# Kernel tuning notes

Hardware: AMD Instinct MI355X
Metric: run time of the kernel (lower is better)

The kernel has to match this reference:

```python
import jax, jax.numpy as jnp
import numpy as np

DIM, DFF, NH = 768, 2048, 12
HD = DIM // NH
N, NOBJ, L = 16, 52, 24
EPS = 1e-5


def setup_inputs() -> dict:
    key = jax.random.key(0)
    ks = jax.random.split(key, 16)
    g = lambda k, shape: jax.random.normal(k, shape, jnp.float32) * 0.02
    inp = {
        "lang": jax.random.normal(ks[0], (N, L, DIM), jnp.float32),
        "obj": jax.random.normal(ks[1], (N, NOBJ, DIM), jnp.float32),
        "lang_mask": jnp.ones((N, L), jnp.int32),
        "obj_mask": jnp.ones((N, NOBJ), jnp.int32),
        "co_mask": jnp.ones((N, L, NOBJ), jnp.int32),
    }
    # two multi-head attention blocks (edge / node): q,k,v,o projections
    for i, nm in enumerate(["e_wq", "e_wk", "e_wv", "e_wo", "n_wq", "n_wk", "n_wv", "n_wo"]):
        inp[nm] = g(ks[2 + i], (DIM, DIM))
        inp[nm.replace("w", "b")] = jnp.zeros((DIM,), jnp.float32)
    inp["ffn_w1"] = g(ks[10], (2 * DIM, DFF)); inp["ffn_b1"] = jnp.zeros((DFF,), jnp.float32)
    inp["ffn_w2"] = g(ks[11], (DFF, DIM)); inp["ffn_b2"] = jnp.zeros((DIM,), jnp.float32)
    for nm in ["ln_e", "ln_q", "ln2"]:
        inp[nm + "_g"] = jnp.ones((DIM,), jnp.float32)
        inp[nm + "_b"] = jnp.zeros((DIM,), jnp.float32)
    return inp


def _layernorm(x, g, b):
    m = jnp.mean(x, -1, keepdims=True)
    v = jnp.mean((x - m) ** 2, -1, keepdims=True)
    return (x - m) * jax.lax.rsqrt(v + EPS) * g + b


def _fwd(lang, obj, co_mask,
         e_wq, e_bq, e_wk, e_bk, e_wv, e_bv, e_wo, e_bo,
         n_wq, n_bq, n_wk, n_bk, n_wv, n_bv, n_wo, n_bo,
         ffn_w1, ffn_b1, ffn_w2, ffn_b2,
         ln_e_g, ln_e_b, ln_q_g, ln_q_b, ln2_g, ln2_b):
    scale = jnp.float32(1.0 / np.sqrt(HD))
    co_t = co_mask.swapaxes(1, 2)  # [N, nobj, L]: query objects attend over lang keys

    # ---- node branch: standard cross-attention obj -> lang ----
    qh = (obj @ n_wq + n_bq).reshape(N, NOBJ, NH, HD)
    kh = (lang @ n_wk + n_bk).reshape(N, L, NH, HD)
    vh = (lang @ n_wv + n_bv).reshape(N, L, NH, HD)
    s = jnp.einsum('nqhd,nlhd->nhql', qh, kh) * scale  # [N,H,nobj,L]
    s = jnp.where(co_t[:, None, :, :] > 0, s, jnp.float32(-1e9))
    a = jax.nn.softmax(s, axis=-1)
    node = jnp.einsum('nhql,nlhd->nqhd', a, vh).reshape(N, NOBJ, DIM) @ n_wo + n_bo

    # ---- edge branch: pairwise diffs attend over lang, then max over partner ----
    diff = obj[:, :, None, :] - obj[:, None, :, :]            # [N,i,j,D]
    qhe = (diff @ e_wq + e_bq).reshape(N, NOBJ, NOBJ, NH, HD)
    khe = (lang @ e_wk + e_bk).reshape(N, L, NH, HD)
    vhe = (lang @ e_wv + e_bv).reshape(N, L, NH, HD)
    se = jnp.einsum('nijhd,nlhd->nhijl', qhe, khe) * scale    # [N,H,i,j,L]
    # mask depends on (n, j, l): torch repeats co_mask^T over the i batch dim
    se = jnp.where(co_t[:, None, None, :, :] > 0, se, jnp.float32(-1e9))
    ae = jax.nn.softmax(se, axis=-1)
    oe = jnp.einsum('nhijl,nlhd->nijhd', ae, vhe).reshape(N, NOBJ, NOBJ, DIM)
    oe = oe @ e_wo + e_bo                                      # [N,i,j,D]
    edge = jnp.max(oe, axis=2)                                 # max over query/partner j -> [N,i,D]

    # ---- fuse ----
    xe = _layernorm(obj + edge, ln_e_g, ln_e_b)
    xn = _layernorm(obj + node, ln_q_g, ln_q_b)
    h = jnp.concatenate((xn, xe), -1)
    h = jax.nn.relu(h @ ffn_w1 + ffn_b1) @ ffn_w2 + ffn_b2
    return _layernorm(xn + h, ln2_g, ln2_b)


def reference(lang, obj, lang_mask, obj_mask, co_mask,
              e_wq, e_bq, e_wk, e_bk, e_wv, e_bv, e_wo, e_bo,
              n_wq, n_bq, n_wk, n_bk, n_wv, n_bv, n_wo, n_bo,
              ffn_w1, ffn_b1, ffn_w2, ffn_b2,
              ln_e_g, ln_e_b, ln_q_g, ln_q_b, ln2_g, ln2_b):
    return _fwd(lang, obj, co_mask,
                e_wq, e_bq, e_wk, e_bk, e_wv, e_bv, e_wo, e_bo,
                n_wq, n_bq, n_wk, n_bk, n_wv, n_bv, n_wo, n_bo,
                ffn_w1, ffn_b1, ffn_w2, ffn_b2,
                ln_e_g, ln_e_b, ln_q_g, ln_q_b, ln2_g, ln2_b)
```

## Files before the change

### kernel.cpp

```cpp
#include <hip/hip_runtime.h>
#include <math.h>

#define NOBJ 52
#define LL 24
#define NHEAD 12

typedef __attribute__((ext_vector_type(8))) short bf16x8;
typedef __attribute__((ext_vector_type(4))) float f32x4;
typedef __attribute__((ext_vector_type(4))) unsigned int u32x4;
typedef __attribute__((ext_vector_type(2))) unsigned int u32x2;

__device__ __forceinline__ unsigned short f2b(float x) {
    union { float f; unsigned int u; } v; v.f = x;
    unsigned int r = v.u + 0x7fffu + ((v.u >> 16) & 1u);
    return (unsigned short)(r >> 16);
}
__device__ __forceinline__ float b2f(unsigned short u) {
    union { unsigned int u; float f; } v; v.u = ((unsigned int)u) << 16;
    return v.f;
}
__device__ __forceinline__ unsigned int pack2(float a, float b) {
    return (unsigned int)f2b(a) | ((unsigned int)f2b(b) << 16);
}
__device__ __forceinline__ f32x4 mfma16(bf16x8 a, bf16x8 b, f32x4 c) {
    return __builtin_amdgcn_mfma_f32_16x16x32_bf16(a, b, c, 0, 0, 0);
}
__device__ __forceinline__ void gl_lds16(const void* g, void* lds) {
    __builtin_amdgcn_global_load_lds(
        (const __attribute__((address_space(1))) unsigned int*)g,
        (__attribute__((address_space(3))) unsigned int*)lds, 16, 0, 0);
}

__device__ __forceinline__ void transpose_tile(const float* __restrict__ src,
    unsigned short* __restrict__ dst, int K, int N, int t, char* smem)
{
    float (*ts)[65] = (float(*)[65])smem;
    const int tid = threadIdx.x;
    const int ntk = K >> 6;
    const int k0 = (t % ntk) << 6, n0 = (t / ntk) << 6;
    const int tx = tid & 63, ty = tid >> 6;
    #pragma unroll
    for (int i2 = 0; i2 < 16; ++i2) {
        const int row = i2 * 4 + ty;
        ts[row][tx] = src[(size_t)(k0 + row) * N + n0 + tx];
    }
    __syncthreads();
    #pragma unroll
    for (int i2 = 0; i2 < 16; ++i2) {
        const int row = i2 * 4 + ty;
        dst[(size_t)(n0 + row) * K + k0 + tx] = f2b(ts[tx][row]);
    }
}

__global__ __launch_bounds__(256)
void pack1_kernel(const float* s0, const float* s1, const float* s2,
                  const float* s3, const float* s4, const float* s5,
                  const float* s6, const float* s7,
                  unsigned short* d0, unsigned short* d1, unsigned short* d2,
                  unsigned short* d3, unsigned short* d4, unsigned short* d5,
                  unsigned short* d6, unsigned short* d7,
                  const float* obj, const float* lang, const float* n_bq,
                  const float* e_bk, const float* e_bv,
                  const float* n_bk, const float* n_bv,
                  unsigned short* objb, unsigned short* langb,
                  float* bqc, float* blc)
{
    __shared__ __align__(16) char smem[16640];
    const int bid = blockIdx.x;
    const int tid = threadIdx.x;
    if (bid < 1152) {
        const int job = bid / 144, t = bid % 144;
        const float* src; unsigned short* dst;
        switch (job) {
            case 0: src = s0; dst = d0; break;
            case 1: src = s1; dst = d1; break;
            case 2: src = s2; dst = d2; break;
            case 3: src = s3; dst = d3; break;
            case 4: src = s4; dst = d4; break;
            case 5: src = s5; dst = d5; break;
            case 6: src = s6; dst = d6; break;
            default: src = s7; dst = d7; break;
        }
        transpose_tile(src, dst, 768, 768, t, smem);
    } else {
        const int base = ((bid - 1152) * 256 + tid) * 4;
        const int T0 = 638976, T1 = 933888, T2 = 935424, T3 = 938496;
        if (base >= T3) return;
        if (base < T0) {
            f32x4 v = *(const f32x4*)(obj + base);
            *(u32x2*)(objb + base) = (u32x2){pack2(v[0], v[1]), pack2(v[2], v[3])};
        } else if (base < T1) {
            const int j = base - T0;
            f32x4 v = *(const f32x4*)(lang + j);
            *(u32x2*)(langb + j) = (u32x2){pack2(v[0], v[1]), pack2(v[2], v[3])};
        } else if (base < T2) {
            const int j = base - T1;
            if (j < 768) { *(f32x4*)(bqc + j) = (f32x4){0.f, 0.f, 0.f, 0.f}; }
            else         { *(f32x4*)(bqc + j) = *(const f32x4*)(n_bq + j - 768); }
        } else {
            const int j = base - T2;
            const int s = j / 768, c = j % 768;
            const float* p = (s == 0) ? e_bk : (s == 1) ? e_bv : (s == 2) ? n_bk : n_bv;
            *(f32x4*)(blc + j) = *(const f32x4*)(p + c);
        }
    }
}

struct GemmJob {
    const unsigned short* A; const unsigned short* Bt; const float* bias;
    float* C; unsigned short* Cb;
    int lda, ldb, ldc, K, nbx, nb, relu, swz;
};

__device__ __forceinline__ void gemm_body(const GemmJob J, int bid, char* smem)
{
    unsigned short* As = (unsigned short*)smem;
    unsigned short* Bs = (unsigned short*)(smem + 16384);
    int bx, by;
    if (J.swz) {
        const int cpx = J.nb >> 3;
        const int gid = (bid & 7) * cpx + (bid >> 3);
        const int nbm = J.nb / J.nbx;
        bx = gid / nbm; by = gid % nbm;
    } else { bx = bid % J.nbx; by = bid / J.nbx; }
    const int n0 = bx * 128, m0 = by * 64;
    const int tid = threadIdx.x;
    const int lane = tid & 63;
    const int w = tid >> 6, wr = w >> 1, wc = w & 1;
    const int lr = lane & 15, lk = lane >> 4;
    const int lda = J.lda, ldb = J.ldb, K = J.K;
    const unsigned short* Ab = J.A + (size_t)m0 * lda;
    const unsigned short* Bb = J.Bt + (size_t)n0 * ldb;

    f32x4 acc[2][4] = {};
    const int NT = K >> 6;

    #pragma unroll
    for (int q = 0; q < 2; ++q) {
        const int c = q * 256 + tid, row = c >> 3, p = (c & 7) ^ (row & 7);
        gl_lds16(Ab + (size_t)row * lda + p * 8, As + c * 8);
    }
    #pragma unroll
    for (int q = 0; q < 4; ++q) {
        const int c = q * 256 + tid, row = c >> 3, p = (c & 7) ^ (row & 7);
        gl_lds16(Bb + (size_t)row * ldb + p * 8, Bs + c * 8);
    }
    __syncthreads();

    for (int t = 0; t < NT; ++t) {
        const int cur = t & 1;
        if (t + 1 < NT) {
            const int k0 = (t + 1) << 6;
            #pragma unroll
            for (int q = 0; q < 2; ++q) {
                const int c = q * 256 + tid, row = c >> 3, p = (c & 7) ^ (row & 7);
                gl_lds16(Ab + (size_t)row * lda + k0 + p * 8, As + (cur ^ 1) * 4096 + c * 8);
            }
            #pragma unroll
            for (int q = 0; q < 4; ++q) {
                const int c = q * 256 + tid, row = c >> 3, p = (c & 7) ^ (row & 7);
                gl_lds16(Bb + (size_t)row * ldb + k0 + p * 8, Bs + (cur ^ 1) * 8192 + c * 8);
            }
        }
        #pragma unroll
        for (int kk = 0; kk < 2; ++kk) {
            bf16x8 af[2], bv[4];
            #pragma unroll
            for (int mt = 0; mt < 2; ++mt) {
                const int row = wr * 32 + mt * 16 + lr;
                const int pc = (kk * 4 + lk) ^ (row & 7);
                af[mt] = *(const bf16x8*)(As + cur * 4096 + row * 64 + pc * 8);
            }
            #pragma unroll
            for (int nt = 0; nt < 4; ++nt) {
                const int col = wc * 64 + nt * 16 + lr;
                const int pc = (kk * 4 + lk) ^ (col & 7);
                bv[nt] = *(const bf16x8*)(Bs + cur * 8192 + col * 64 + pc * 8);
            }
            #pragma unroll
            for (int mt = 0; mt < 2; ++mt)
                #pragma unroll
                for (int nt = 0; nt < 4; ++nt)
                    acc[mt][nt] = mfma16(af[mt], bv[nt], acc[mt][nt]);
        }
        __syncthreads();
    }

    #pragma unroll
    for (int mt = 0; mt < 2; ++mt) {
        #pragma unroll
        for (int nt = 0; nt < 4; ++nt) {
            const int col = n0 + wc * 64 + nt * 16 + lr;
            const float bvv = J.bias ? J.bias[col] : 0.f;
            #pragma unroll
            for (int r = 0; r < 4; ++r) {
                const int row = m0 + wr * 32 + mt * 16 + lk * 4 + r;
                float v = acc[mt][nt][r] + bvv;
                if (J.relu) v = fmaxf(v, 0.f);
                if (J.C)  J.C[(size_t)row * J.ldc + col] = v;
                if (J.Cb) J.Cb[(size_t)row * J.ldc + col] = f2b(v);
            }
        }
    }
}

__global__ __launch_bounds__(256)
void gemm_tn4(GemmJob j0, GemmJob j1, GemmJob j2, GemmJob j3)
{
    __shared__ __align__(16) char smem[49152];
    int bid = blockIdx.x;
    if (bid < j0.nb) { gemm_body(j0, bid, smem); return; }
    bid -= j0.nb;
    if (bid < j1.nb) { gemm_body(j1, bid, smem); return; }
    bid -= j1.nb;
    if (bid < j2.nb) { gemm_body(j2, bid, smem); return; }
    bid -= j2.nb;
    gemm_body(j3, bid, smem);
}

__global__ __launch_bounds__(256)
void proj_pack_kernel(GemmJob j0, GemmJob j1,
                      const float* w1, const float* w2,
                      unsigned short* W1t, unsigned short* W2t)
{
    __shared__ __align__(16) char smem[49152];
    int bid = blockIdx.x;
    if (bid < j0.nb) { gemm_body(j0, bid, smem); return; }
    bid -= j0.nb;
    if (bid < j1.nb) { gemm_body(j1, bid, smem); return; }
    const int t = bid - j1.nb;
    if (t < 768) transpose_tile(w1, W1t, 1536, 2048, t, smem);
    else transpose_tile(w2, W2t, 2048, 768, t - 768, smem);
}

__global__ __launch_bounds__(256)
void mid3_kernel(const unsigned short* __restrict__ QCb,
                 const unsigned short* __restrict__ LCb,
                 const unsigned short* __restrict__ Wet,
                 const unsigned short* __restrict__ Wot,
                 const float* __restrict__ e_bq,
                 unsigned short* __restrict__ VWe,
                 unsigned short* __restrict__ VWn,
                 float* __restrict__ S2e, float* __restrict__ Tb,
                 float* __restrict__ S2n)
{
    __shared__ __align__(16) union USm {
        struct { unsigned short As[8192], Bs[8192]; } g;
        unsigned short Ct[128 * 136];
        struct { float sA[52][68], sB[24][68]; } s;
    } U;
    const int bid = blockIdx.x;
    const int tid = threadIdx.x;

    if (bid < 432) {
        const int sub = bid >= 216;
        const int b = sub ? bid - 216 : bid;
        const int aoff = sub ? 2304 : 768;
        const unsigned short* Bt = sub ? Wot : Wet;
        unsigned short* Vout = sub ? VWn : VWe;

        const int h = b / 18, rm = b % 18, mt = rm / 6, ntile = rm % 6;
        const int m0 = mt * 128, n0 = ntile * 128;
        const int lane = tid & 63, w = tid >> 6, wr = w >> 1, wc = w & 1;
        const int lr = lane & 15, lk = lane >> 4;
        #pragma unroll
        for (int q = 0; q < 4; ++q) {
            const int c = q * 256 + tid, row = c >> 3, p = (c & 7) ^ (row & 7);
            gl_lds16(LCb + (size_t)(m0 + row) * 3072 + aoff + h * 64 + p * 8, &U.g.As[c * 8]);
            gl_lds16(Bt + (size_t)(n0 + row) * 768 + h * 64 + p * 8, &U.g.Bs[c * 8]);
        }
        __syncthreads();
        f32x4 acc[4][4] = {};
        #pragma unroll
        for (int kk = 0; kk < 2; ++kk) {
            bf16x8 af[4], bv[4];
            #pragma unroll
            for (int m2 = 0; m2 < 4; ++m2) {
                const int row = wr * 64 + m2 * 16 + lr;
                const int pc = (kk * 4 + lk) ^ (row & 7);
                af[m2] = *(const bf16x8*)&U.g.As[row * 64 + pc * 8];
            }
            #pragma unroll
            for (int n2 = 0; n2 < 4; ++n2) {
                const int col = wc * 64 + n2 * 16 + lr;
                const int pc = (kk * 4 + lk) ^ (col & 7);
                bv[n2] = *(const bf16x8*)&U.g.Bs[col * 64 + pc * 8];
            }
            #pragma unroll
            for (int m2 = 0; m2 < 4; ++m2)
                #pragma unroll
                for (int n2 = 0; n2 < 4; ++n2)
                    acc[m2][n2] = mfma16(af[m2], bv[n2], acc[m2][n2]);
        }
        __syncthreads();
        #pragma unroll
        for (int m2 = 0; m2 < 4; ++m2)
            #pragma unroll
            for (int n2 = 0; n2 < 4; ++n2) {
                const int col = wc * 64 + n2 * 16 + lr;
                #pragma unroll
                for (int r = 0; r < 4; ++r) {
                    const int row = wr * 64 + m2 * 16 + lk * 4 + r;
                    U.Ct[row * 136 + col] = f2b(acc[m2][n2][r]);
                }
            }
        __syncthreads();
        #pragma unroll
        for (int q = 0; q < 8; ++q) {
            const int item = q * 256 + tid;
            const int dl = item & 127, kg = item >> 7;
            const int m = m0 + kg * 8;
            const int nn = m / 24, l0 = m % 24;
            const int kc = (h * 24 + l0) >> 3;
            const int ks = kc >> 2;
            const int dg = n0 + dl;
            const int kpos = (kc & 3) ^ ((dg >> 1) & 3);
            u32x4 uu;
            #pragma unroll
            for (int e = 0; e < 4; ++e)
                uu[e] = (unsigned int)U.Ct[(kg * 8 + 2 * e) * 136 + dl]
                      | ((unsigned int)U.Ct[(kg * 8 + 2 * e + 1) * 136 + dl] << 16);
            *(u32x4*)(Vout + (size_t)nn * 221184 + ks * 24576 + dg * 32 + kpos * 8) = uu;
        }
    } else {
        const int sub = bid >= 624;
        const int b = bid - (sub ? 624 : 432);
        const int n = b / NHEAD, h = b % NHEAD;
        const int qoff = sub ? 768 : 0, koff = sub ? 1536 : 0;
        float* Sout = sub ? S2n : S2e;
        for (int p = tid; p < 52 * 64; p += 256) {
            const int q = p >> 6, d = p & 63;
            U.s.sA[q][d] = b2f(QCb[(size_t)(n * 52 + q) * 1536 + qoff + h * 64 + d]);
        }
        for (int p = tid; p < 24 * 64; p += 256) {
            const int l = p >> 6, d = p & 63;
            U.s.sB[l][d] = b2f(LCb[(size_t)(n * 24 + l) * 3072 + koff + h * 64 + d]);
        }
        __syncthreads();
        for (int p = tid; p < 52 * 24; p += 256) {
            const int q = p / 24, l = p % 24;
            float s = 0.f;
            #pragma unroll
            for (int d = 0; d < 64; ++d) s += U.s.sA[q][d] * U.s.sB[l][d];
            Sout[((size_t)(n * NHEAD + h) * 52 + q) * 24 + l] = s;
        }
        if (!sub && tid < 24) {
            float s = 0.f;
            #pragma unroll
            for (int d = 0; d < 64; ++d) s += e_bq[h * 64 + d] * U.s.sB[tid][d];
            Tb[((size_t)n * NHEAD + h) * 24 + tid] = s;
        }
    }
}

__global__ __launch_bounds__(512)
void attn_kernel(const float* __restrict__ S2e, const float* __restrict__ Tb,
                 const float* __restrict__ S2n, const int* __restrict__ co_mask,
                 const unsigned short* __restrict__ VWe,
                 const unsigned short* __restrict__ VWn,
                 const float* __restrict__ ebo, const float* __restrict__ nbo,
                 unsigned short* __restrict__ EdgeBb,
                 unsigned short* __restrict__ NodePb)
{
    __shared__ __align__(16) char smem[126464];
    unsigned short* Pf = (unsigned short*)smem;
    unsigned short* Bs = (unsigned short*)(smem + 73728);
    float* SiT = (float*)(smem + 122880);
    unsigned char* cmb = (unsigned char*)(smem + 125184);
    const int bid = blockIdx.x;
    const int tid = threadIdx.x;
    const int lane = tid & 63, w = tid >> 6;
    const int lr = lane & 15, lk = lane >> 4;

    if (bid < 832) {
        const int sw = (bid & 7) * 104 + (bid >> 3);
        const int n = sw / 52;
        const int r52 = sw % 52;
        const int ip = r52 >> 1, dh = r52 & 1;
        const int i0 = ip * 2;
        const unsigned short* Bsrc = VWe + (size_t)n * 221184 + dh * 12288;
        const float* S2x = S2e + (size_t)n * NHEAD * 52 * 24;

        #pragma unroll
        for (int q = 0; q < 3; ++q) {
            const int c = q * 512 + tid;
            gl_lds16(Bsrc + c * 8, Bs + c * 8);
        }
        for (int p = tid; p < 576; p += 512) {
            const int ii = p >= 288 ? 1 : 0;
            const int rl = p - ii * 288;
            const int h = rl / 24, l = rl % 24;
            SiT[ii * 288 + rl] = S2x[((size_t)h * 52 + i0 + ii) * 24 + l]
                               + Tb[((size_t)n * NHEAD + h) * 24 + l];
        }
        for (int p = tid; p < 1248; p += 512)
            cmb[p] = (unsigned char)(co_mask[(size_t)n * 1248 + p] > 0);
        __syncthreads();

        for (int p = tid; p < 1248; p += 512) {
            const int ii = p >= 624 ? 1 : 0;
            const int rl = p - ii * 624;
            const int h = rl / 52, j = rl % 52;
            const float* Sj = S2x + ((size_t)h * 52 + j) * 24;
            const float* st = SiT + ii * 288 + h * 24;
            float x[24]; float mx = -1e30f;
            #pragma unroll
            for (int l = 0; l < 24; ++l) {
                float v = (st[l] - Sj[l]) * 0.125f;
                v = cmb[l * 52 + j] ? v : -1e9f;
                x[l] = v; mx = fmaxf(mx, v);
            }
            float sum = 0.f;
            #pragma unroll
            for (int l = 0; l < 24; ++l) { const float e = __expf(x[l] - mx); x[l] = e; sum += e; }
            const float inv = 1.f / sum;
            unsigned short* Prow = Pf + ii * 18432 + j * 288;
            const int swk = (j >> 1) & 3;
            #pragma unroll
            for (int c = 0; c < 3; ++c) {
                u32x4 u;
                #pragma unroll
                for (int m = 0; m < 4; ++m)
                    u[m] = pack2(x[c * 8 + 2 * m] * inv, x[c * 8 + 2 * m + 1] * inv);
                *(u32x4*)(Prow + (((3 * h + c) ^ swk) << 3)) = u;
            }
        }
        __syncthreads();

        const int iw = w >> 2, cg = (w & 3) * 96;
        f32x4 acc[4][6] = {};
        for (int ks = 0; ks < 9; ++ks) {
            const int cur = ks & 1;
            if (ks < 8) {
                const unsigned short* src = Bsrc + (size_t)(ks + 1) * 24576;
                #pragma unroll
                for (int q = 0; q < 3; ++q) {
                    const int c = q * 512 + tid;
                    gl_lds16(src + c * 8, Bs + (cur ^ 1) * 12288 + c * 8);
                }
            }
            bf16x8 af[4];
            #pragma unroll
            for (int mt = 0; mt < 4; ++mt) {
                const int row = mt * 16 + lr;
                af[mt] = *(const bf16x8*)(Pf + iw * 18432 + row * 288
                                          + (((ks * 4 + lk) ^ ((row >> 1) & 3)) << 3));
            }
            #pragma unroll
            for (int nt = 0; nt < 6; ++nt) {
                const int cl = cg + nt * 16 + lr;
                bf16x8 bv = *(const bf16x8*)(Bs + cur * 12288 + cl * 32
                                             + ((lk ^ ((cl >> 1) & 3)) << 3));
                #pragma unroll
                for (int mt = 0; mt < 4; ++mt)
                    acc[mt][nt] = mfma16(af[mt], bv, acc[mt][nt]);
            }
            __syncthreads();
        }

        #pragma unroll
        for (int nt = 0; nt < 6; ++nt) {
            float m = -1e30f;
            #pragma unroll
            for (int mt = 0; mt < 4; ++mt)
                #pragma unroll
                for (int r = 0; r < 4; ++r) {
                    const int row = mt * 16 + lk * 4 + r;
                    if (row < NOBJ) m = fmaxf(m, acc[mt][nt][r]);
                }
            m = fmaxf(m, __shfl_xor(m, 16));
            m = fmaxf(m, __shfl_xor(m, 32));
            if (lk == 0) {
                const int col = dh * 384 + cg + nt * 16 + lr;
                EdgeBb[(size_t)(n * 52 + i0 + iw) * 768 + col] = f2b(m + ebo[col]);
            }
        }
    } else {
        const int t = bid - 832;
        const int n = t >> 1, dh = t & 1;
        const unsigned short* Bsrc = VWn + (size_t)n * 221184 + dh * 12288;
        const float* S2x = S2n + (size_t)n * NHEAD * 52 * 24;

        #pragma unroll
        for (int q = 0; q < 3; ++q) {
            const int c = q * 512 + tid;
            gl_lds16(Bsrc + c * 8, Bs + c * 8);
        }
        for (int p = tid; p < 1248; p += 512)
            cmb[p] = (unsigned char)(co_mask[(size_t)n * 1248 + p] > 0);
        __syncthreads();

        for (int p = tid; p < 624; p += 512) {
            const int h = p / 52, q = p % 52;
            const float* Sq = S2x + ((size_t)h * 52 + q) * 24;
            float x[24]; float mx = -1e30f;
            #pragma unroll
            for (int l = 0; l < 24; ++l) {
                float v = Sq[l] * 0.125f;
                v = cmb[l * 52 + q] ? v : -1e9f;
                x[l] = v; mx = fmaxf(mx, v);
            }
            float sum = 0.f;
            #pragma unroll
            for (int l = 0; l < 24; ++l) { const float e = __expf(x[l] - mx); x[l] = e; sum += e; }
            const float inv = 1.f / sum;
            unsigned short* Prow = Pf + q * 288;
            const int swk = (q >> 1) & 3;
            #pragma unroll
            for (int c = 0; c < 3; ++c) {
                u32x4 u;
                #pragma unroll
                for (int m = 0; m < 4; ++m)
                    u[m] = pack2(x[c * 8 + 2 * m] * inv, x[c * 8 + 2 * m + 1] * inv);
                *(u32x4*)(Prow + (((3 * h + c) ^ swk) << 3)) = u;
            }
        }
        __syncthreads();

        const int cg = w * 48;
        f32x4 acc[4][3] = {};
        for (int ks = 0; ks < 9; ++ks) {
            const int cur = ks & 1;
            if (ks < 8) {
                const unsigned short* src = Bsrc + (size_t)(ks + 1) * 24576;
                #pragma unroll
                for (int q = 0; q < 3; ++q) {
                    const int c = q * 512 + tid;
                    gl_lds16(src + c * 8, Bs + (cur ^ 1) * 12288 + c * 8);
                }
            }
            bf16x8 af[4];
            #pragma unroll
            for (int mt = 0; mt < 4; ++mt) {
                const int row = mt * 16 + lr;
                af[mt] = *(const bf16x8*)(Pf + row * 288
                                          + (((ks * 4 + lk) ^ ((row >> 1) & 3)) << 3));
            }
            #pragma unroll
            for (int nt = 0; nt < 3; ++nt) {
                const int cl = cg + nt * 16 + lr;
                bf16x8 bv = *(const bf16x8*)(Bs + cur * 12288 + cl * 32
                                             + ((lk ^ ((cl >> 1) & 3)) << 3));
                #pragma unroll
                for (int mt = 0; mt < 4; ++mt)
                    acc[mt][nt] = mfma16(af[mt], bv, acc[mt][nt]);
            }
            __syncthreads();
        }

        #pragma unroll
        for (int nt = 0; nt < 3; ++nt) {
            const int col = dh * 384 + cg + nt * 16 + lr;
            const float bv = nbo[col];
            #pragma unroll
            for (int mt = 0; mt < 4; ++mt)
                #pragma unroll
                for (int r = 0; r < 4; ++r) {
                    const int row = mt * 16 + lk * 4 + r;
                    if (row < NOBJ)
                        NodePb[(size_t)(n * 52 + row) * 768 + col] = f2b(acc[mt][nt][r] + bv);
                }
        }
    }
}

__global__ __launch_bounds__(256)
void ln_dual_kernel(const float* __restrict__ obj,
                    const unsigned short* __restrict__ NodePb,
                    const unsigned short* __restrict__ EdgeBb,
                    const float* __restrict__ gq, const float* __restrict__ bq,
                    const float* __restrict__ ge, const float* __restrict__ be,
                    unsigned short* __restrict__ Fusedb)
{
    __shared__ float red[8];
    const int job = blockIdx.x >= 832;
    const int row = blockIdx.x - (job ? 832 : 0);
    const int tid = threadIdx.x;
    const unsigned short* x2 = (job ? EdgeBb : NodePb) + (size_t)row * 768;
    const float* x1 = obj + (size_t)row * 768;
    const float* g = job ? ge : gq;
    const float* bb = job ? be : bq;
    float v[3]; float s = 0.f;
    #pragma unroll
    for (int c = 0; c < 3; ++c) {
        const int col = tid + 256 * c;
        v[c] = x1[col] + b2f(x2[col]); s += v[c];
    }
    #pragma unroll
    for (int o = 32; o; o >>= 1) s += __shfl_xor(s, o);
    if ((tid & 63) == 0) red[tid >> 6] = s;
    __syncthreads();
    const float mean = (red[0] + red[1] + red[2] + red[3]) * (1.f / 768.f);
    float var = 0.f;
    #pragma unroll
    for (int c = 0; c < 3; ++c) { const float d = v[c] - mean; var += d * d; }
    #pragma unroll
    for (int o = 32; o; o >>= 1) var += __shfl_xor(var, o);
    __syncthreads();
    if ((tid & 63) == 0) red[4 + (tid >> 6)] = var;
    __syncthreads();
    const float vt = (red[4] + red[5] + red[6] + red[7]) * (1.f / 768.f);
    const float rs = rsqrtf(vt + 1e-5f);
    unsigned short* dst = Fusedb + (size_t)row * 1536 + (job ? 768 : 0);
    #pragma unroll
    for (int c = 0; c < 3; ++c) {
        const int col = tid + 256 * c;
        dst[col] = f2b((v[c] - mean) * rs * g[col] + bb[col]);
    }
}

__global__ __launch_bounds__(256)
void ln2_kernel(const unsigned short* __restrict__ x1b,
                const float* __restrict__ Hp, const float* __restrict__ b2,
                const float* __restrict__ g, const float* __restrict__ bb,
                float* __restrict__ dst)
{
    __shared__ float red[8];
    const int row = blockIdx.x, tid = threadIdx.x;
    float v[3]; float s = 0.f;
    #pragma unroll
    for (int c = 0; c < 3; ++c) {
        const int col = tid + 256 * c;
        const size_t o = (size_t)row * 768 + col;
        float h = Hp[o] + Hp[638976 + o] + Hp[2 * 638976 + o] + Hp[3 * 638976 + o];
        v[c] = b2f(x1b[(size_t)row * 1536 + col]) + h + b2[col];
        s += v[c];
    }
    #pragma unroll
    for (int o = 32; o; o >>= 1) s += __shfl_xor(s, o);
    if ((tid & 63) == 0) red[tid >> 6] = s;
    __syncthreads();
    const float mean = (red[0] + red[1] + red[2] + red[3]) * (1.f / 768.f);
    float var = 0.f;
    #pragma unroll
    for (int c = 0; c < 3; ++c) { const float d = v[c] - mean; var += d * d; }
    #pragma unroll
    for (int o = 32; o; o >>= 1) var += __shfl_xor(var, o);
    __syncthreads();
    if ((tid & 63) == 0) red[4 + (tid >> 6)] = var;
    __syncthreads();
    const float vt = (red[4] + red[5] + red[6] + red[7]) * (1.f / 768.f);
    const float rs = rsqrtf(vt + 1e-5f);
    #pragma unroll
    for (int c = 0; c < 3; ++c) {
        const int col = tid + 256 * c;
        dst[(size_t)row * 768 + col] = (v[c] - mean) * rs * g[col] + bb[col];
    }
}

extern "C" void kernel_launch(void* const* d_in, const int* in_sizes, int n_in,
                              void* d_out, int out_size, void* d_ws, size_t ws_size,
                              hipStream_t stream)
{
    (void)in_sizes; (void)n_in; (void)out_size; (void)ws_size;
    const float* lang  = (const float*)d_in[0];
    const float* obj   = (const float*)d_in[1];
    const int* co_mask = (const int*)d_in[4];
    const float* e_wq = (const float*)d_in[5];
    const float* e_bq = (const float*)d_in[6];
    const float* e_wk = (const float*)d_in[7];
    const float* e_bk = (const float*)d_in[8];
    const float* e_wv = (const float*)d_in[9];
    const float* e_bv = (const float*)d_in[10];
    const float* e_wo = (const float*)d_in[11];
    const float* e_bo = (const float*)d_in[12];
    const float* n_wq = (const float*)d_in[13];
    const float* n_bq = (const float*)d_in[14];
    const float* n_wk = (const float*)d_in[15];
    const float* n_bk = (const float*)d_in[16];
    const float* n_wv = (const float*)d_in[17];
    const float* n_bv = (const float*)d_in[18];
    const float* n_wo = (const float*)d_in[19];
    const float* n_bo = (const float*)d_in[20];
    const float* ffn_w1 = (const float*)d_in[21];
    const float* ffn_b1 = (const float*)d_in[22];
    const float* ffn_w2 = (const float*)d_in[23];
    const float* ffn_b2 = (const float*)d_in[24];
    const float* ln_e_g = (const float*)d_in[25];
    const float* ln_e_b = (const float*)d_in[26];
    const float* ln_q_g = (const float*)d_in[27];
    const float* ln_q_b = (const float*)d_in[28];
    const float* ln2_g = (const float*)d_in[29];
    const float* ln2_b = (const float*)d_in[30];
    float* out = (float*)d_out;

    char* wsb = (char*)d_ws;
    unsigned short* Wqt   = (unsigned short*)(wsb + 0);
    unsigned short* Wlt   = (unsigned short*)(wsb + 2359296);
    unsigned short* Wet   = (unsigned short*)(wsb + 7077888);
    unsigned short* Wot   = (unsigned short*)(wsb + 8257536);
    unsigned short* W1t   = (unsigned short*)(wsb + 9437184);
    unsigned short* W2t   = (unsigned short*)(wsb + 15728640);
    unsigned short* objb  = (unsigned short*)(wsb + 18874368);
    unsigned short* langb = (unsigned short*)(wsb + 20152320);
    float*          bqc   = (float*)(wsb + 20742144);
    float*          blc   = (float*)(wsb + 20748288);
    unsigned short* QCb   = (unsigned short*)(wsb + 20760576);
    unsigned short* LCb   = (unsigned short*)(wsb + 23316480);
    float*          S2e   = (float*)(wsb + 25675776);
    float*          Tb    = (float*)(wsb + 26634240);
    float*          S2n   = (float*)(wsb + 26652672);
    unsigned short* VWe   = (unsigned short*)(wsb + 27611136);
    unsigned short* VWn   = (unsigned short*)(wsb + 34689024);
    unsigned short* NodePb= (unsigned short*)(wsb + 41766912);
    unsigned short* EdgeBb= (unsigned short*)(wsb + 43044864);
    unsigned short* Fusedb= (unsigned short*)(wsb + 44322816);
    unsigned short* H1b   = (unsigned short*)(wsb + 46878720);
    float*          Hp    = (float*)(wsb + 50286592);

    dim3 blk(256);
    pack1_kernel<<<2069, blk, 0, stream>>>(
        e_wq, n_wq, e_wk, e_wv, n_wk, n_wv, n_wo, e_wo,
        Wqt, Wqt + 589824, Wlt, Wlt + 589824, Wlt + 2 * 589824, Wlt + 3 * 589824,
        Wot, Wet,
        obj, lang, n_bq, e_bk, e_bv, n_bk, n_bv, objb, langb, bqc, blc);
    {
        GemmJob p0 = {objb, Wqt, bqc, nullptr, QCb, 768, 768, 1536, 768, 12, 156, 0, 0};
        GemmJob p1 = {langb, Wlt, blc, nullptr, LCb, 768, 768, 3072, 768, 24, 144, 0, 0};
        proj_pack_kernel<<<1452, blk, 0, stream>>>(p0, p1, ffn_w1, ffn_w2, W1t, W2t);
    }
    mid3_kernel<<<816, blk, 0, stream>>>(QCb, LCb, Wet, Wot, e_bq,
                                         VWe, VWn, S2e, Tb, S2n);
    attn_kernel<<<864, dim3(512), 0, stream>>>(S2e, Tb, S2n, co_mask, VWe, VWn,
                                               e_bo, n_bo, EdgeBb, NodePb);
    ln_dual_kernel<<<1664, blk, 0, stream>>>(obj, NodePb, EdgeBb, ln_q_g, ln_q_b,
                                             ln_e_g, ln_e_b, Fusedb);
    {
        GemmJob p0 = {Fusedb, W1t, ffn_b1, nullptr, H1b, 1536, 1536, 2048, 1536, 16, 208, 1, 1};
        gemm_tn4<<<208, blk, 0, stream>>>(p0, p0, p0, p0);
    }
    {
        GemmJob q0 = {H1b,        W2t,        nullptr, Hp,               nullptr, 2048, 2048, 768, 512, 6, 78, 0, 0};
        GemmJob q1 = {H1b + 512,  W2t + 512,  nullptr, Hp + 638976,      nullptr, 2048, 2048, 768, 512, 6, 78, 0, 0};
        GemmJob q2 = {H1b + 1024, W2t + 1024, nullptr, Hp + 2 * 638976,  nullptr, 2048, 2048, 768, 512, 6, 78, 0, 0};
        GemmJob q3 = {H1b + 1536, W2t + 1536, nullptr, Hp + 3 * 638976,  nullptr, 2048, 2048, 768, 512, 6, 78, 0, 0};
        gemm_tn4<<<312, blk, 0, stream>>>(q0, q1, q2, q3);
    }
    ln2_kernel<<<832, blk, 0, stream>>>(Fusedb, Hp, ffn_b2, ln2_g, ln2_b, out);
}
```

Baseline: 126.8 us.

## Split attention kernel into smaller blocks with single-buffered LDS and transposed scores

```diff
diff --git a/kernel.cpp b/kernel.cpp
--- a/kernel.cpp
+++ b/kernel.cpp
@@ -247,7 +247,7 @@
     __shared__ __align__(16) union USm {
         struct { unsigned short As[8192], Bs[8192]; } g;
         unsigned short Ct[128 * 136];
-        struct { float sA[52][68], sB[24][68]; } s;
+        struct { float sA[52][65], sB[24][65]; } s;
     } U;
     const int bid = blockIdx.x;
     const int tid = threadIdx.x;
@@ -338,11 +338,11 @@
         }
         __syncthreads();
         for (int p = tid; p < 52 * 24; p += 256) {
-            const int q = p / 24, l = p % 24;
+            const int l = p / 52, q = p % 52;
             float s = 0.f;
             #pragma unroll
             for (int d = 0; d < 64; ++d) s += U.s.sA[q][d] * U.s.sB[l][d];
-            Sout[((size_t)(n * NHEAD + h) * 52 + q) * 24 + l] = s;
+            Sout[((size_t)(n * NHEAD + h) * 24 + l) * 52 + q] = s;
         }
         if (!sub && tid < 24) {
             float s = 0.f;
@@ -353,7 +353,7 @@
     }
 }
 
-__global__ __launch_bounds__(512)
+__global__ __launch_bounds__(256)
 void attn_kernel(const float* __restrict__ S2e, const float* __restrict__ Tb,
                  const float* __restrict__ S2n, const int* __restrict__ co_mask,
                  const unsigned short* __restrict__ VWe,
@@ -362,51 +362,50 @@
                  unsigned short* __restrict__ EdgeBb,
                  unsigned short* __restrict__ NodePb)
 {
-    __shared__ __align__(16) char smem[126464];
+    __shared__ __align__(16) char smem[75776];
     unsigned short* Pf = (unsigned short*)smem;
-    unsigned short* Bs = (unsigned short*)(smem + 73728);
-    float* SiT = (float*)(smem + 122880);
-    unsigned char* cmb = (unsigned char*)(smem + 125184);
+    unsigned short* Bs = (unsigned short*)(smem + 59904);
+    float* SiT = (float*)(smem + 72192);
+    unsigned char* cmb = (unsigned char*)(smem + 74496);
     const int bid = blockIdx.x;
     const int tid = threadIdx.x;
     const int lane = tid & 63, w = tid >> 6;
     const int lr = lane & 15, lk = lane >> 4;
 
-    if (bid < 832) {
-        const int sw = (bid & 7) * 104 + (bid >> 3);
-        const int n = sw / 52;
-        const int r52 = sw % 52;
-        const int ip = r52 >> 1, dh = r52 & 1;
+    if (bid < 1664) {
+        const int sw = (bid & 7) * 208 + (bid >> 3);
+        const int n = sw / 104;
+        const int r104 = sw % 104;
+        const int ip = r104 >> 2, dq = r104 & 3;
         const int i0 = ip * 2;
-        const unsigned short* Bsrc = VWe + (size_t)n * 221184 + dh * 12288;
-        const float* S2x = S2e + (size_t)n * NHEAD * 52 * 24;
+        const unsigned short* Bsrc = VWe + (size_t)n * 221184 + dq * 6144;
+        const float* S2x = S2e + (size_t)n * NHEAD * 24 * 52;
 
         #pragma unroll
         for (int q = 0; q < 3; ++q) {
-            const int c = q * 512 + tid;
+            const int c = q * 256 + tid;
             gl_lds16(Bsrc + c * 8, Bs + c * 8);
         }
-        for (int p = tid; p < 576; p += 512) {
+        for (int p = tid; p < 576; p += 256) {
             const int ii = p >= 288 ? 1 : 0;
             const int rl = p - ii * 288;
-            const int h = rl / 24, l = rl % 24;
-            SiT[ii * 288 + rl] = S2x[((size_t)h * 52 + i0 + ii) * 24 + l]
-                               + Tb[((size_t)n * NHEAD + h) * 24 + l];
-        }
-        for (int p = tid; p < 1248; p += 512)
+            SiT[ii * 288 + rl] = S2x[(size_t)rl * 52 + i0 + ii]
+                               + Tb[(size_t)n * 288 + rl];
+        }
+        for (int p = tid; p < 1248; p += 256)
             cmb[p] = (unsigned char)(co_mask[(size_t)n * 1248 + p] > 0);
         __syncthreads();
 
-        for (int p = tid; p < 1248; p += 512) {
+        for (int p = tid; p < 1248; p += 256) {
             const int ii = p >= 624 ? 1 : 0;
             const int rl = p - ii * 624;
             const int h = rl / 52, j = rl % 52;
-            const float* Sj = S2x + ((size_t)h * 52 + j) * 24;
+            const float* Sc = S2x + (size_t)h * 24 * 52 + j;
             const float* st = SiT + ii * 288 + h * 24;
             float x[24]; float mx = -1e30f;
             #pragma unroll
             for (int l = 0; l < 24; ++l) {
-                float v = (st[l] - Sj[l]) * 0.125f;
+                float v = (st[l] - Sc[l * 52]) * 0.125f;
                 v = cmb[l * 52 + j] ? v : -1e9f;
                 x[l] = v; mx = fmaxf(mx, v);
             }
@@ -414,7 +413,7 @@
             #pragma unroll
             for (int l = 0; l < 24; ++l) { const float e = __expf(x[l] - mx); x[l] = e; sum += e; }
             const float inv = 1.f / sum;
-            unsigned short* Prow = Pf + ii * 18432 + j * 288;
+            unsigned short* Prow = Pf + ii * 14976 + j * 288;
             const int swk = (j >> 1) & 3;
             #pragma unroll
             for (int c = 0; c < 3; ++c) {
@@ -427,35 +426,36 @@
         }
         __syncthreads();
 
-        const int iw = w >> 2, cg = (w & 3) * 96;
+        const int iw = w >> 1, cg = (w & 1) * 96;
         f32x4 acc[4][6] = {};
         for (int ks = 0; ks < 9; ++ks) {
-            const int cur = ks & 1;
-            if (ks < 8) {
-                const unsigned short* src = Bsrc + (size_t)(ks + 1) * 24576;
-                #pragma unroll
-                for (int q = 0; q < 3; ++q) {
-                    const int c = q * 512 + tid;
-                    gl_lds16(src + c * 8, Bs + (cur ^ 1) * 12288 + c * 8);
-                }
-            }
             bf16x8 af[4];
             #pragma unroll
             for (int mt = 0; mt < 4; ++mt) {
                 const int row = mt * 16 + lr;
-                af[mt] = *(const bf16x8*)(Pf + iw * 18432 + row * 288
-                                          + (((ks * 4 + lk) ^ ((row >> 1) & 3)) << 3));
+                const int rowc = row < NOBJ ? row : 0;
+                af[mt] = *(const bf16x8*)(Pf + iw * 14976 + rowc * 288
+                                          + (((ks * 4 + lk) ^ ((rowc >> 1) & 3)) << 3));
             }
             #pragma unroll
             for (int nt = 0; nt < 6; ++nt) {
                 const int cl = cg + nt * 16 + lr;
-                bf16x8 bv = *(const bf16x8*)(Bs + cur * 12288 + cl * 32
+                bf16x8 bv = *(const bf16x8*)(Bs + cl * 32
                                              + ((lk ^ ((cl >> 1) & 3)) << 3));
                 #pragma unroll
                 for (int mt = 0; mt < 4; ++mt)
                     acc[mt][nt] = mfma16(af[mt], bv, acc[mt][nt]);
             }
-            __syncthreads();
+            if (ks < 8) {
+                __syncthreads();
+                const unsigned short* src = Bsrc + (size_t)(ks + 1) * 24576;
+                #pragma unroll
+                for (int q = 0; q < 3; ++q) {
+                    const int c = q * 256 + tid;
+                    gl_lds16(src + c * 8, Bs + c * 8);
+                }
+                __syncthreads();
+            }
         }
 
         #pragma unroll
@@ -471,32 +471,32 @@
             m = fmaxf(m, __shfl_xor(m, 16));
             m = fmaxf(m, __shfl_xor(m, 32));
             if (lk == 0) {
-                const int col = dh * 384 + cg + nt * 16 + lr;
+                const int col = dq * 192 + cg + nt * 16 + lr;
                 EdgeBb[(size_t)(n * 52 + i0 + iw) * 768 + col] = f2b(m + ebo[col]);
             }
         }
     } else {
-        const int t = bid - 832;
-        const int n = t >> 1, dh = t & 1;
-        const unsigned short* Bsrc = VWn + (size_t)n * 221184 + dh * 12288;
-        const float* S2x = S2n + (size_t)n * NHEAD * 52 * 24;
+        const int t = bid - 1664;
+        const int n = t >> 2, dq = t & 3;
+        const unsigned short* Bsrc = VWn + (size_t)n * 221184 + dq * 6144;
+        const float* S2x = S2n + (size_t)n * NHEAD * 24 * 52;
 
         #pragma unroll
         for (int q = 0; q < 3; ++q) {
-            const int c = q * 512 + tid;
+            const int c = q * 256 + tid;
             gl_lds16(Bsrc + c * 8, Bs + c * 8);
         }
-        for (int p = tid; p < 1248; p += 512)
+        for (int p = tid; p < 1248; p += 256)
             cmb[p] = (unsigned char)(co_mask[(size_t)n * 1248 + p] > 0);
         __syncthreads();
 
-        for (int p = tid; p < 624; p += 512) {
+        for (int p = tid; p < 624; p += 256) {
             const int h = p / 52, q = p % 52;
-            const float* Sq = S2x + ((size_t)h * 52 + q) * 24;
+            const float* Sc = S2x + (size_t)h * 24 * 52 + q;
             float x[24]; float mx = -1e30f;
             #pragma unroll
             for (int l = 0; l < 24; ++l) {
-                float v = Sq[l] * 0.125f;
+                float v = Sc[l * 52] * 0.125f;
                 v = cmb[l * 52 + q] ? v : -1e9f;
                 x[l] = v; mx = fmaxf(mx, v);
             }
@@ -520,37 +520,38 @@
         const int cg = w * 48;
         f32x4 acc[4][3] = {};
         for (int ks = 0; ks < 9; ++ks) {
-            const int cur = ks & 1;
-            if (ks < 8) {
-                const unsigned short* src = Bsrc + (size_t)(ks + 1) * 24576;
-                #pragma unroll
-                for (int q = 0; q < 3; ++q) {
-                    const int c = q * 512 + tid;
-                    gl_lds16(src + c * 8, Bs + (cur ^ 1) * 12288 + c * 8);
-                }
-            }
             bf16x8 af[4];
             #pragma unroll
             for (int mt = 0; mt < 4; ++mt) {
                 const int row = mt * 16 + lr;
-                af[mt] = *(const bf16x8*)(Pf + row * 288
-                                          + (((ks * 4 + lk) ^ ((row >> 1) & 3)) << 3));
+                const int rowc = row < NOBJ ? row : 0;
+                af[mt] = *(const bf16x8*)(Pf + rowc * 288
+                                          + (((ks * 4 + lk) ^ ((rowc >> 1) & 3)) << 3));
             }
             #pragma unroll
             for (int nt = 0; nt < 3; ++nt) {
                 const int cl = cg + nt * 16 + lr;
-                bf16x8 bv = *(const bf16x8*)(Bs + cur * 12288 + cl * 32
+                bf16x8 bv = *(const bf16x8*)(Bs + cl * 32
                                              + ((lk ^ ((cl >> 1) & 3)) << 3));
                 #pragma unroll
                 for (int mt = 0; mt < 4; ++mt)
                     acc[mt][nt] = mfma16(af[mt], bv, acc[mt][nt]);
             }
-            __syncthreads();
+            if (ks < 8) {
+                __syncthreads();
+                const unsigned short* src = Bsrc + (size_t)(ks + 1) * 24576;
+                #pragma unroll
+                for (int q = 0; q < 3; ++q) {
+                    const int c = q * 256 + tid;
+                    gl_lds16(src + c * 8, Bs + c * 8);
+                }
+                __syncthreads();
+            }
         }
 
         #pragma unroll
         for (int nt = 0; nt < 3; ++nt) {
-            const int col = dh * 384 + cg + nt * 16 + lr;
+            const int col = dq * 192 + cg + nt * 16 + lr;
             const float bv = nbo[col];
             #pragma unroll
             for (int mt = 0; mt < 4; ++mt)
@@ -721,8 +722,8 @@
     }
     mid3_kernel<<<816, blk, 0, stream>>>(QCb, LCb, Wet, Wot, e_bq,
                                          VWe, VWn, S2e, Tb, S2n);
-    attn_kernel<<<864, dim3(512), 0, stream>>>(S2e, Tb, S2n, co_mask, VWe, VWn,
-                                               e_bo, n_bo, EdgeBb, NodePb);
+    attn_kernel<<<1728, blk, 0, stream>>>(S2e, Tb, S2n, co_mask, VWe, VWn,
+                                          e_bo, n_bo, EdgeBb, NodePb);
     ln_dual_kernel<<<1664, blk, 0, stream>>>(obj, NodePb, EdgeBb, ln_q_g, ln_q_b,
                                              ln_e_g, ln_e_b, Fusedb);
     {
```

Result: slower. 143.2 us (+12.9%).
